# Kernel optimization log

Measured on AMD Instinct MI355X. Metric: run time of the kernel, lower is better.

## Reference

```python
import jax, jax.numpy as jnp
import numpy as np

G = 64        # supervoxel grid per dim (cfg.orig_grid_shape)
CELL = 16     # pixels per grid cell
T = 32        # tile size in px (covers 2x2 cells)
NT = 32       # tiles per dim per shift config
CH = 40       # Conv_trio channels


def setup_inputs() -> dict:
    key = jax.random.key(0)
    ks = jax.random.split(key, 8)
    W = G * CELL
    curr_image = jax.random.normal(ks[0], (W, W), jnp.float32)
    # masks encode per-pixel supervoxel id (pixel belongs to cell floor(px/CELL))
    ids = (jnp.arange(G)[:, None] * G + jnp.arange(G)[None, :]).astype(jnp.float32)
    masks = jnp.repeat(jnp.repeat(ids, CELL, axis=0), CELL, axis=1)[..., None]
    return {
        'curr_image': curr_image,
        'masks': masks,
        'conv1_w': jax.random.normal(ks[1], (3, 3, 1, CH), jnp.float32) * 0.1,
        'conv1_b': jnp.zeros((CH,), jnp.float32),
        'ln1_s': jnp.ones((CH,), jnp.float32),
        'ln1_b': jnp.zeros((CH,), jnp.float32),
        'conv2_w': jax.random.normal(ks[2], (3, 3, CH, CH), jnp.float32) * 0.1,
        'conv2_b': jnp.zeros((CH,), jnp.float32),
        'ln2_s': jnp.ones((CH,), jnp.float32),
        'ln2_b': jnp.zeros((CH,), jnp.float32),
        'dense_w': jax.random.normal(ks[3], ((T // 4) * (T // 4) * CH, 6), jnp.float32) * 0.02,
        'dense_b': jnp.zeros((6,), jnp.float32),
    }


def _tile(a):
    # [W, W, c] -> [NT*NT, T, T, c]
    c = a.shape[-1]
    return a.reshape(NT, T, NT, T, c).transpose(0, 2, 1, 3, 4).reshape(NT * NT, T, T, c)


def _config_tokens(img, masks, ids, sx, sy):
    # shifted tiling: tile (i,j) covers px [T*i + sx*CELL, ...)
    rolled_img = jnp.roll(img, (-sx * CELL, -sy * CELL), (0, 1))
    rolled_msk = jnp.roll(masks, (-sx * CELL, -sy * CELL), (0, 1))
    img_t = _tile(rolled_img)          # [NT*NT, T, T, 1]
    msk_t = _tile(rolled_msk)[..., 0]  # [NT*NT, T, T]
    curr_ids = ids[sx::2, sy::2].reshape(-1)  # [NT*NT]
    filt = (msk_t == curr_ids[:, None, None]).astype(img_t.dtype)
    return img_t * filt[..., None]


def _conv_trio(x, w, b, s, bln):
    y = jax.lax.conv_general_dilated(x, w, (2, 2), 'SAME',
                                     dimension_numbers=('NHWC', 'HWIO', 'NHWC')) + b
    mu = jnp.mean(y, axis=-1, keepdims=True)
    var = jnp.var(y, axis=-1, keepdims=True)
    y = (y - mu) * jax.lax.rsqrt(var + 1e-6) * s + bln
    return jax.nn.gelu(y)


def reference(curr_image, masks, conv1_w, conv1_b, ln1_s, ln1_b,
              conv2_w, conv2_b, ln2_s, ln2_b, dense_w, dense_b):
    img = curr_image[..., None]  # [W, W, 1]
    ids = (jnp.arange(G)[:, None] * G + jnp.arange(G)[None, :]).astype(masks.dtype)
    tokens = jnp.concatenate([
        _config_tokens(img, masks, ids, 0, 0),
        _config_tokens(img, masks, ids, 1, 0),
        _config_tokens(img, masks, ids, 0, 1),
        _config_tokens(img, masks, ids, 1, 1),
    ], axis=0)  # [4*NT*NT, T, T, 1]
    x = _conv_trio(tokens, conv1_w, conv1_b, ln1_s, ln1_b)  # [F, 16, 16, 40]
    x = _conv_trio(x, conv2_w, conv2_b, ln2_s, ln2_b)       # [F, 8, 8, 40]
    x = x.reshape(x.shape[0], -1)
    return x @ dense_w + dense_b  # node embeddings [F, 6]
```

## Files before the change

### kernel.cpp

```cpp
#include <hip/hip_runtime.h>
#include <math.h>

#define CH 40
#define IMW 1024
#define TOKH (9*10*40)
#define W2T_HALVES (48*48*8)
#define Z1_OFF W2T_HALVES
#define OUTC_OFF (Z1_OFF + 40)
#define Y2T 768

typedef _Float16 v8h __attribute__((ext_vector_type(8)));
typedef _Float16 v4h __attribute__((ext_vector_type(4)));
typedef float    v4f __attribute__((ext_vector_type(4)));
typedef float    v2f __attribute__((ext_vector_type(2)));

__device__ __forceinline__ float gelu_fast(float x) {
    float u = 1.5957691216057308f * (x + 0.044715f * x * x * x);
    return x * __builtin_amdgcn_rcpf(1.0f + __expf(-u));
}

__global__ __launch_bounds__(256) void prep_kernel(
    const float* __restrict__ w2,
    const float* __restrict__ b1, const float* __restrict__ s1,
    const float* __restrict__ bb1,
    const float* __restrict__ b2, const float* __restrict__ s2,
    const float* __restrict__ bb2,
    const float* __restrict__ dw, const float* __restrict__ db,
    _Float16* __restrict__ ws)
{
    const int t = threadIdx.x;
    int idx0 = blockIdx.x * 256 + t;
    for (int idx = idx0; idx < W2T_HALVES; idx += gridDim.x * 256) {
        int j   = idx & 7;
        int co  = (idx >> 3) % 48;
        int kgg = idx / (48 * 8);
        int k   = kgg * 8 + j;
        float v = 0.0f;
        if (co < CH && k < 360) {
            int wi = k / 40, ci = k - wi * 40;
            v = w2[(wi * CH + ci) * CH + co];
        }
        ws[idx] = (_Float16)v;
    }
    if (blockIdx.x != 0) return;

    __shared__ float zs[40];
    __shared__ float w2sum[9][40];
    __shared__ float p2l[120];
    __shared__ float red[4][6];

    if (t < 120) p2l[t] = (t < 40) ? b2[t] : (t < 80 ? s2[t - 40] : bb2[t - 80]);

    if (t >= 64 && t < 128) {
        int lane = t - 64;
        bool act = lane < CH;
        float bv = act ? b1[lane] : 0.f;
        float s = bv;
        #pragma unroll
        for (int m = 1; m < 64; m <<= 1) s += __shfl_xor(s, m, 64);
        float mu = s * (1.0f / CH);
        float d = act ? (bv - mu) : 0.f;
        float q = d * d;
        #pragma unroll
        for (int m = 1; m < 64; m <<= 1) q += __shfl_xor(q, m, 64);
        float rs = rsqrtf(q * (1.0f / CH) + 1e-6f);
        if (act) {
            float g = gelu_fast((bv - mu) * rs * s1[lane] + bb1[lane]);
            zs[lane] = g;
            ws[Z1_OFF + lane] = (_Float16)g;
        }
    }
    __syncthreads();

    for (int idx = t; idx < 360; idx += 256) {
        int wi = idx / 40, ch = idx - wi * 40;
        float s = 0.f;
        #pragma unroll
        for (int ci = 0; ci < CH; ci++)
            s += w2[(wi * CH + ci) * CH + ch] * zs[ci];
        w2sum[wi][ch] = s;
    }
    __syncthreads();

    {
        const int m = t >> 2, sub = t & 3;
        const int p = m >> 3, q = m & 7;
        const int co0 = sub * 10;
        float a6[6] = {0.f, 0.f, 0.f, 0.f, 0.f, 0.f};
        if (p >= 4 || q >= 4) {
            const int drmax = (p == 7) ? 2 : 3;
            const int dcmax = (q == 7) ? 2 : 3;
            float vv[10];
            float s_own = 0.f;
            #pragma unroll
            for (int u = 0; u < 10; u++) {
                float v = p2l[co0 + u];
                for (int dr = 0; dr < drmax; dr++)
                    for (int dc = 0; dc < dcmax; dc++)
                        v += w2sum[dr * 3 + dc][co0 + u];
                vv[u] = v; s_own += v;
            }
            s_own += __shfl_xor(s_own, 1, 64);
            s_own += __shfl_xor(s_own, 2, 64);
            float mu = s_own * (1.0f / CH);
            float v_own = 0.f;
            #pragma unroll
            for (int u = 0; u < 10; u++) { float d = vv[u] - mu; v_own += d * d; }
            v_own += __shfl_xor(v_own, 1, 64);
            v_own += __shfl_xor(v_own, 2, 64);
            float rs = rsqrtf(v_own * (1.0f / CH) + 1e-6f);
            const float* wp = &dw[(m * CH + co0) * 6];
            #pragma unroll
            for (int u = 0; u < 10; u++) {
                float gv = gelu_fast((vv[u] - mu) * rs * p2l[40 + co0 + u] + p2l[80 + co0 + u]);
                v2f w01 = *(const v2f*)&wp[u * 6];
                v2f w23 = *(const v2f*)&wp[u * 6 + 2];
                v2f w45 = *(const v2f*)&wp[u * 6 + 4];
                a6[0] += gv * w01[0]; a6[1] += gv * w01[1];
                a6[2] += gv * w23[0]; a6[3] += gv * w23[1];
                a6[4] += gv * w45[0]; a6[5] += gv * w45[1];
            }
        }
        #pragma unroll
        for (int off = 32; off > 0; off >>= 1)
            #pragma unroll
            for (int k = 0; k < 6; k++) a6[k] += __shfl_down(a6[k], off, 64);
        int wv = t >> 6, lane = t & 63;
        if (lane == 0) {
            #pragma unroll
            for (int k = 0; k < 6; k++) red[wv][k] = a6[k];
        }
        __syncthreads();
        if (t == 0) {
            float* oc = (float*)&ws[OUTC_OFF];
            #pragma unroll
            for (int k = 0; k < 6; k++)
                oc[k] = red[0][k] + red[1][k] + red[2][k] + red[3][k] + db[k];
        }
    }
}

__global__ __launch_bounds__(256) void sgn_kernel(
    const float* __restrict__ img,
    const float* __restrict__ w1, const float* __restrict__ b1,
    const float* __restrict__ s1, const float* __restrict__ bb1,
    const float* __restrict__ b2, const float* __restrict__ s2,
    const float* __restrict__ bb2,
    const float* __restrict__ dw,
    const _Float16* __restrict__ ws,
    float* __restrict__ out)
{
    __shared__ __align__(16) unsigned char sbuf[2 * TOKH * 2];
    _Float16* x1h = (_Float16*)sbuf;
    float*    y2f = (float*)sbuf;
    __shared__ float img_s[2][16][16];
    __shared__ float w1t[40 * 12];
    __shared__ float p1s[120];
    __shared__ float p2s[120];
    __shared__ unsigned koff_s[48];

    const int t = threadIdx.x;

    int crr[2], ccc[2];
    #pragma unroll
    for (int tk = 0; tk < 2; tk++) {
        int f   = blockIdx.x * 2 + tk;
        int cfg = f >> 10;
        int ij  = f & 1023;
        int ti  = ij >> 5, tj = ij & 31;
        crr[tk] = 2 * ti + (cfg & 1);
        ccc[tk] = 2 * tj + (cfg >> 1);
    }

    {
        int r = t >> 4, c = t & 15;
        #pragma unroll
        for (int tk = 0; tk < 2; tk++)
            img_s[tk][r][c] = img[(crr[tk] * 16 + r) * IMW + ccc[tk] * 16 + c];
    }
    for (int i = t; i < 360; i += 256) {
        int k = i / 40, ch = i - k * 40;
        w1t[ch * 12 + k] = w1[i];
    }
    if (t < 120) {
        p1s[t] = (t < 40) ? b1[t] : (t < 80 ? s1[t - 40] : bb1[t - 80]);
    } else if (t >= 128 && t < 248) {
        int i = t - 128;
        p2s[i] = (i < 40) ? b2[i] : (i < 80 ? s2[i - 40] : bb2[i - 80]);
    }
    if (t < 48) {
        int s = t >> 2, kg = t & 3;
        int k0 = 32 * s + 8 * kg;
        unsigned v = 0;
        if (k0 < 360) {
            int wi = k0 / 40, ci0 = k0 - wi * 40;
            int dr = wi / 3, dc = wi - 3 * dr;
            v = (unsigned)((dr * 10 + dc) * 40 + ci0);
        }
        koff_s[t] = v;
    }
    __syncthreads();

    {
        const int tk  = t >> 7;
        const int pos = (t >> 1) & 63;
        const int sub = t & 1;
        const int r = pos >> 3, c = pos & 7;
        float vin[9];
        #pragma unroll
        for (int dr = 0; dr < 3; dr++)
            #pragma unroll
            for (int dc = 0; dc < 3; dc++) {
                int rr = 2 * r + dr, cp = 2 * c + dc;
                vin[dr * 3 + dc] = (rr < 16 && cp < 16) ? img_s[tk][rr][cp] : 0.0f;
            }
        const int ch0 = sub * 20;
        float y[20];
        float s_own = 0.f;
        #pragma unroll
        for (int u = 0; u < 20; u++) {
            float a = p1s[ch0 + u];
            const float* wr = &w1t[(ch0 + u) * 12];
            #pragma unroll
            for (int k = 0; k < 9; k++) a += vin[k] * wr[k];
            y[u] = a; s_own += a;
        }
        s_own += __shfl_xor(s_own, 1, 64);
        float mu = s_own * (1.0f / CH);
        float v_own = 0.f;
        #pragma unroll
        for (int u = 0; u < 20; u++) { float d = y[u] - mu; v_own += d * d; }
        v_own += __shfl_xor(v_own, 1, 64);
        float rs = rsqrtf(v_own * (1.0f / CH) + 1e-6f);
        _Float16 g[20];
        #pragma unroll
        for (int u = 0; u < 20; u++) {
            int ch = ch0 + u;
            g[u] = (_Float16)gelu_fast((y[u] - mu) * rs * p1s[40 + ch] + p1s[80 + ch]);
        }
        const int base = tk * TOKH + (r * 10 + c) * 40 + ch0;
        if (sub == 0) {
            *(v8h*)&x1h[base]      = *(v8h*)&g[0];
            *(v8h*)&x1h[base + 8]  = *(v8h*)&g[8];
            *(v4h*)&x1h[base + 16] = *(v4h*)&g[16];
        } else {
            *(v4h*)&x1h[base]      = *(v4h*)&g[0];
            *(v8h*)&x1h[base + 4]  = *(v8h*)&g[4];
            *(v8h*)&x1h[base + 12] = *(v8h*)&g[12];
        }
    }
    if (t < 34) {
        int tk = (t >= 17), i = t - tk * 17;
        int r = (i < 9) ? 8 : (i - 9);
        int c = (i < 9) ? i : 8;
        const v8h* zsrc = (const v8h*)&ws[Z1_OFF];
        int base = tk * TOKH + (r * 10 + c) * 40;
        *(v8h*)&x1h[base]      = zsrc[0];
        *(v8h*)&x1h[base + 8]  = zsrc[1];
        *(v8h*)&x1h[base + 16] = zsrc[2];
        *(v8h*)&x1h[base + 24] = zsrc[3];
        *(v8h*)&x1h[base + 32] = zsrc[4];
    }
    __syncthreads();

    v4f accA = {0,0,0,0}, accB = {0,0,0,0};
    const int wv   = t >> 6;
    const int lane = t & 63;
    if (wv < 3) {
        const int row = lane & 15;
        const int kg  = lane >> 4;
        const unsigned pbase = (unsigned)((20 * (row >> 2) + 2 * (row & 3)) * 40);
        #pragma unroll
        for (int s = 0; s < 12; s++) {
            const int kc = (s << 2) | kg;
            unsigned aoff = pbase + koff_s[kc];
            v8h a0 = *(const v8h*)&x1h[aoff];
            v8h a1 = *(const v8h*)&x1h[TOKH + aoff];
            v8h bf = *(const v8h*)&ws[(kc * 48 + wv * 16 + row) * 8];
            accA = __builtin_amdgcn_mfma_f32_16x16x32_f16(a0, bf, accA, 0, 0, 0);
            accB = __builtin_amdgcn_mfma_f32_16x16x32_f16(a1, bf, accB, 0, 0, 0);
        }
    }
    __syncthreads();

    if (wv < 3) {
        const int cix = lane & 15;
        const int kg  = lane >> 4;
        if (wv < 2 || cix < 8) {
            #pragma unroll
            for (int j = 0; j < 4; j++) {
                int m = (kg << 2) | j;
                y2f[m * 48 + wv * 16 + cix]       = accA[j];
                y2f[Y2T + m * 48 + wv * 16 + cix] = accB[j];
            }
        }
    }
    __syncthreads();

    if (t < 128) {
        const int tk  = t >> 6;
        const int pos = (t >> 2) & 15;
        const int sub = t & 3;
        const int co0 = sub * 10;
        float vv[10];
        float s_own = 0.f;
        #pragma unroll
        for (int u = 0; u < 10; u++) {
            float a = y2f[tk * Y2T + pos * 48 + co0 + u] + p2s[co0 + u];
            vv[u] = a; s_own += a;
        }
        s_own += __shfl_xor(s_own, 1, 64);
        s_own += __shfl_xor(s_own, 2, 64);
        float mu = s_own * (1.0f / CH);
        float v_own = 0.f;
        #pragma unroll
        for (int u = 0; u < 10; u++) { float d = vv[u] - mu; v_own += d * d; }
        v_own += __shfl_xor(v_own, 1, 64);
        v_own += __shfl_xor(v_own, 2, 64);
        float rs = rsqrtf(v_own * (1.0f / CH) + 1e-6f);

        const int p = pos >> 2, q = pos & 3;
        const float* wp = &dw[((p * 8 + q) * CH + co0) * 6];
        float a6[6] = {0.f, 0.f, 0.f, 0.f, 0.f, 0.f};
        #pragma unroll
        for (int u = 0; u < 10; u++) {
            float gv = gelu_fast((vv[u] - mu) * rs * p2s[40 + co0 + u] + p2s[80 + co0 + u]);
            v2f w01 = *(const v2f*)&wp[u * 6];
            v2f w23 = *(const v2f*)&wp[u * 6 + 2];
            v2f w45 = *(const v2f*)&wp[u * 6 + 4];
            a6[0] += gv * w01[0]; a6[1] += gv * w01[1];
            a6[2] += gv * w23[0]; a6[3] += gv * w23[1];
            a6[4] += gv * w45[0]; a6[5] += gv * w45[1];
        }
        #pragma unroll
        for (int off = 32; off > 0; off >>= 1)
            #pragma unroll
            for (int k = 0; k < 6; k++) a6[k] += __shfl_down(a6[k], off, 64);
        if (lane == 0) {
            const float* oc = (const float*)&ws[OUTC_OFF];
            int f = blockIdx.x * 2 + tk;
            #pragma unroll
            for (int k = 0; k < 6; k++) out[f * 6 + k] = a6[k] + oc[k];
        }
    }
}

extern "C" void kernel_launch(void* const* d_in, const int* in_sizes, int n_in,
                              void* d_out, int out_size, void* d_ws, size_t ws_size,
                              hipStream_t stream) {
    const float* img = (const float*)d_in[0];
    const float* w1  = (const float*)d_in[2];
    const float* b1  = (const float*)d_in[3];
    const float* s1  = (const float*)d_in[4];
    const float* bb1 = (const float*)d_in[5];
    const float* w2  = (const float*)d_in[6];
    const float* b2  = (const float*)d_in[7];
    const float* s2  = (const float*)d_in[8];
    const float* bb2 = (const float*)d_in[9];
    const float* dw  = (const float*)d_in[10];
    const float* db  = (const float*)d_in[11];
    float* out = (float*)d_out;
    _Float16* ws = (_Float16*)d_ws;

    prep_kernel<<<32, 256, 0, stream>>>(w2, b1, s1, bb1, b2, s2, bb2, dw, db, ws);
    sgn_kernel<<<2048, 256, 0, stream>>>(img, w1, b1, s1, bb1,
                                         b2, s2, bb2, dw, ws, out);
}
```

Baseline: 32.21 us.

## Process one token per single-wavefront block with register-resident epilogue

Changes sgn_kernel from 256-thread blocks handling two tokens to 64-thread blocks, one wavefront per token. Each lane now computes all 40 conv1 channels for one output pixel and reads the image straight from global memory instead of staging it in LDS. That wave then issues three MFMAs per K step, one per output-channel group. The conv2 LayerNorm, GELU and dense epilogue work directly on the MFMA accumulators using cross-lane shuffles, which drops the LDS round trip and two block barriers. In exchange, each lane holds more registers (40-channel arrays) and per-block setup (weight and parameter loads into LDS) is repeated twice as often.

```diff
diff --git a/kernel.cpp b/kernel.cpp
--- a/kernel.cpp
+++ b/kernel.cpp
@@ -7,10 +7,8 @@
 #define W2T_HALVES (48*48*8)
 #define Z1_OFF W2T_HALVES
 #define OUTC_OFF (Z1_OFF + 40)
-#define Y2T 768
 
 typedef _Float16 v8h __attribute__((ext_vector_type(8)));
-typedef _Float16 v4h __attribute__((ext_vector_type(4)));
 typedef float    v4f __attribute__((ext_vector_type(4)));
 typedef float    v2f __attribute__((ext_vector_type(2)));
 
@@ -140,7 +138,7 @@
     }
 }
 
-__global__ __launch_bounds__(256) void sgn_kernel(
+__global__ __launch_bounds__(64) void sgn_kernel(
     const float* __restrict__ img,
     const float* __restrict__ w1, const float* __restrict__ b1,
     const float* __restrict__ s1, const float* __restrict__ bb1,
@@ -150,111 +148,83 @@
     const _Float16* __restrict__ ws,
     float* __restrict__ out)
 {
-    __shared__ __align__(16) unsigned char sbuf[2 * TOKH * 2];
-    _Float16* x1h = (_Float16*)sbuf;
-    float*    y2f = (float*)sbuf;
-    __shared__ float img_s[2][16][16];
+    __shared__ __align__(16) _Float16 x1h[TOKH];
     __shared__ float w1t[40 * 12];
     __shared__ float p1s[120];
     __shared__ float p2s[120];
     __shared__ unsigned koff_s[48];
 
-    const int t = threadIdx.x;
-
-    int crr[2], ccc[2];
-    #pragma unroll
-    for (int tk = 0; tk < 2; tk++) {
-        int f   = blockIdx.x * 2 + tk;
-        int cfg = f >> 10;
-        int ij  = f & 1023;
-        int ti  = ij >> 5, tj = ij & 31;
-        crr[tk] = 2 * ti + (cfg & 1);
-        ccc[tk] = 2 * tj + (cfg >> 1);
-    }
-
-    {
-        int r = t >> 4, c = t & 15;
-        #pragma unroll
-        for (int tk = 0; tk < 2; tk++)
-            img_s[tk][r][c] = img[(crr[tk] * 16 + r) * IMW + ccc[tk] * 16 + c];
-    }
-    for (int i = t; i < 360; i += 256) {
+    const int lane = threadIdx.x;
+    const int f   = blockIdx.x;
+    const int cfg = f >> 10;
+    const int ij  = f & 1023;
+    const int ti  = ij >> 5, tj = ij & 31;
+    const int cr  = 2 * ti + (cfg & 1);
+    const int cc  = 2 * tj + (cfg >> 1);
+
+    for (int i = lane; i < 360; i += 64) {
         int k = i / 40, ch = i - k * 40;
         w1t[ch * 12 + k] = w1[i];
     }
-    if (t < 120) {
-        p1s[t] = (t < 40) ? b1[t] : (t < 80 ? s1[t - 40] : bb1[t - 80]);
-    } else if (t >= 128 && t < 248) {
-        int i = t - 128;
+    for (int i = lane; i < 120; i += 64)
+        p1s[i] = (i < 40) ? b1[i] : (i < 80 ? s1[i - 40] : bb1[i - 80]);
+    for (int i = lane; i < 120; i += 64)
         p2s[i] = (i < 40) ? b2[i] : (i < 80 ? s2[i - 40] : bb2[i - 80]);
-    }
-    if (t < 48) {
-        int s = t >> 2, kg = t & 3;
-        int k0 = 32 * s + 8 * kg;
+    if (lane < 48) {
+        int k0 = 8 * lane;
         unsigned v = 0;
         if (k0 < 360) {
             int wi = k0 / 40, ci0 = k0 - wi * 40;
             int dr = wi / 3, dc = wi - 3 * dr;
             v = (unsigned)((dr * 10 + dc) * 40 + ci0);
         }
-        koff_s[t] = v;
+        koff_s[lane] = v;
     }
     __syncthreads();
 
     {
-        const int tk  = t >> 7;
-        const int pos = (t >> 1) & 63;
-        const int sub = t & 1;
-        const int r = pos >> 3, c = pos & 7;
+        const int r = lane >> 3, c = lane & 7;
+        const float* ib = &img[(cr * 16) * IMW + cc * 16];
         float vin[9];
         #pragma unroll
         for (int dr = 0; dr < 3; dr++)
             #pragma unroll
             for (int dc = 0; dc < 3; dc++) {
                 int rr = 2 * r + dr, cp = 2 * c + dc;
-                vin[dr * 3 + dc] = (rr < 16 && cp < 16) ? img_s[tk][rr][cp] : 0.0f;
+                vin[dr * 3 + dc] = (rr < 16 && cp < 16) ? ib[rr * IMW + cp] : 0.0f;
             }
-        const int ch0 = sub * 20;
-        float y[20];
-        float s_own = 0.f;
-        #pragma unroll
-        for (int u = 0; u < 20; u++) {
-            float a = p1s[ch0 + u];
-            const float* wr = &w1t[(ch0 + u) * 12];
+        float y[40];
+        float s = 0.f;
+        #pragma unroll
+        for (int ch = 0; ch < 40; ch++) {
+            float a = p1s[ch];
+            const float* wr = &w1t[ch * 12];
             #pragma unroll
             for (int k = 0; k < 9; k++) a += vin[k] * wr[k];
-            y[u] = a; s_own += a;
-        }
-        s_own += __shfl_xor(s_own, 1, 64);
-        float mu = s_own * (1.0f / CH);
-        float v_own = 0.f;
-        #pragma unroll
-        for (int u = 0; u < 20; u++) { float d = y[u] - mu; v_own += d * d; }
-        v_own += __shfl_xor(v_own, 1, 64);
-        float rs = rsqrtf(v_own * (1.0f / CH) + 1e-6f);
-        _Float16 g[20];
-        #pragma unroll
-        for (int u = 0; u < 20; u++) {
-            int ch = ch0 + u;
-            g[u] = (_Float16)gelu_fast((y[u] - mu) * rs * p1s[40 + ch] + p1s[80 + ch]);
-        }
-        const int base = tk * TOKH + (r * 10 + c) * 40 + ch0;
-        if (sub == 0) {
-            *(v8h*)&x1h[base]      = *(v8h*)&g[0];
-            *(v8h*)&x1h[base + 8]  = *(v8h*)&g[8];
-            *(v4h*)&x1h[base + 16] = *(v4h*)&g[16];
-        } else {
-            *(v4h*)&x1h[base]      = *(v4h*)&g[0];
-            *(v8h*)&x1h[base + 4]  = *(v8h*)&g[4];
-            *(v8h*)&x1h[base + 12] = *(v8h*)&g[12];
-        }
-    }
-    if (t < 34) {
-        int tk = (t >= 17), i = t - tk * 17;
-        int r = (i < 9) ? 8 : (i - 9);
-        int c = (i < 9) ? i : 8;
+            y[ch] = a; s += a;
+        }
+        float mu = s * (1.0f / CH);
+        float q = 0.f;
+        #pragma unroll
+        for (int ch = 0; ch < 40; ch++) { float d = y[ch] - mu; q += d * d; }
+        float rs = rsqrtf(q * (1.0f / CH) + 1e-6f);
+        const int base = (r * 10 + c) * 40;
+        #pragma unroll
+        for (int chk = 0; chk < 5; chk++) {
+            v8h hv;
+            #pragma unroll
+            for (int jj = 0; jj < 8; jj++) {
+                int ch = chk * 8 + jj;
+                hv[jj] = (_Float16)gelu_fast((y[ch] - mu) * rs * p1s[40 + ch] + p1s[80 + ch]);
+            }
+            *(v8h*)&x1h[base + chk * 8] = hv;
+        }
+    }
+    if (lane < 17) {
+        int rr = (lane < 9) ? 8 : (lane - 9);
+        int cb = (lane < 9) ? lane : 8;
         const v8h* zsrc = (const v8h*)&ws[Z1_OFF];
-        int base = tk * TOKH + (r * 10 + c) * 40;
+        int base = (rr * 10 + cb) * 40;
         *(v8h*)&x1h[base]      = zsrc[0];
         *(v8h*)&x1h[base + 8]  = zsrc[1];
         *(v8h*)&x1h[base + 16] = zsrc[2];
@@ -263,74 +233,62 @@
     }
     __syncthreads();
 
-    v4f accA = {0,0,0,0}, accB = {0,0,0,0};
-    const int wv   = t >> 6;
-    const int lane = t & 63;
-    if (wv < 3) {
-        const int row = lane & 15;
-        const int kg  = lane >> 4;
+    v4f acc0 = {0,0,0,0}, acc1 = {0,0,0,0}, acc2 = {0,0,0,0};
+    const int row = lane & 15;
+    const int kg  = lane >> 4;
+    {
         const unsigned pbase = (unsigned)((20 * (row >> 2) + 2 * (row & 3)) * 40);
         #pragma unroll
         for (int s = 0; s < 12; s++) {
             const int kc = (s << 2) | kg;
             unsigned aoff = pbase + koff_s[kc];
-            v8h a0 = *(const v8h*)&x1h[aoff];
-            v8h a1 = *(const v8h*)&x1h[TOKH + aoff];
-            v8h bf = *(const v8h*)&ws[(kc * 48 + wv * 16 + row) * 8];
-            accA = __builtin_amdgcn_mfma_f32_16x16x32_f16(a0, bf, accA, 0, 0, 0);
-            accB = __builtin_amdgcn_mfma_f32_16x16x32_f16(a1, bf, accB, 0, 0, 0);
-        }
-    }
-    __syncthreads();
-
-    if (wv < 3) {
-        const int cix = lane & 15;
-        const int kg  = lane >> 4;
-        if (wv < 2 || cix < 8) {
-            #pragma unroll
-            for (int j = 0; j < 4; j++) {
-                int m = (kg << 2) | j;
-                y2f[m * 48 + wv * 16 + cix]       = accA[j];
-                y2f[Y2T + m * 48 + wv * 16 + cix] = accB[j];
-            }
-        }
-    }
-    __syncthreads();
-
-    if (t < 128) {
-        const int tk  = t >> 6;
-        const int pos = (t >> 2) & 15;
-        const int sub = t & 3;
-        const int co0 = sub * 10;
-        float vv[10];
-        float s_own = 0.f;
-        #pragma unroll
-        for (int u = 0; u < 10; u++) {
-            float a = y2f[tk * Y2T + pos * 48 + co0 + u] + p2s[co0 + u];
-            vv[u] = a; s_own += a;
-        }
-        s_own += __shfl_xor(s_own, 1, 64);
-        s_own += __shfl_xor(s_own, 2, 64);
-        float mu = s_own * (1.0f / CH);
-        float v_own = 0.f;
-        #pragma unroll
-        for (int u = 0; u < 10; u++) { float d = vv[u] - mu; v_own += d * d; }
-        v_own += __shfl_xor(v_own, 1, 64);
-        v_own += __shfl_xor(v_own, 2, 64);
-        float rs = rsqrtf(v_own * (1.0f / CH) + 1e-6f);
-
-        const int p = pos >> 2, q = pos & 3;
-        const float* wp = &dw[((p * 8 + q) * CH + co0) * 6];
+            v8h a = *(const v8h*)&x1h[aoff];
+            const _Float16* wb = &ws[(kc * 48 + row) * 8];
+            v8h bf0 = *(const v8h*)&wb[0];
+            v8h bf1 = *(const v8h*)&wb[16 * 8];
+            v8h bf2 = *(const v8h*)&wb[32 * 8];
+            acc0 = __builtin_amdgcn_mfma_f32_16x16x32_f16(a, bf0, acc0, 0, 0, 0);
+            acc1 = __builtin_amdgcn_mfma_f32_16x16x32_f16(a, bf1, acc1, 0, 0, 0);
+            acc2 = __builtin_amdgcn_mfma_f32_16x16x32_f16(a, bf2, acc2, 0, 0, 0);
+        }
+    }
+
+    {
+        const int cix = row;
+        const bool h2 = (cix < 8);
+        const float b2a = p2s[cix],      b2b = p2s[16 + cix],      b2c = h2 ? p2s[32 + cix] : 0.f;
+        const float s2a = p2s[40 + cix], s2b = p2s[56 + cix],      s2c = h2 ? p2s[72 + cix] : 0.f;
+        const float g2a = p2s[80 + cix], g2b = p2s[96 + cix],      g2c = h2 ? p2s[112 + cix] : 0.f;
         float a6[6] = {0.f, 0.f, 0.f, 0.f, 0.f, 0.f};
         #pragma unroll
-        for (int u = 0; u < 10; u++) {
-            float gv = gelu_fast((vv[u] - mu) * rs * p2s[40 + co0 + u] + p2s[80 + co0 + u]);
-            v2f w01 = *(const v2f*)&wp[u * 6];
-            v2f w23 = *(const v2f*)&wp[u * 6 + 2];
-            v2f w45 = *(const v2f*)&wp[u * 6 + 4];
-            a6[0] += gv * w01[0]; a6[1] += gv * w01[1];
-            a6[2] += gv * w23[0]; a6[3] += gv * w23[1];
-            a6[4] += gv * w45[0]; a6[5] += gv * w45[1];
+        for (int j = 0; j < 4; j++) {
+            const int m = (kg << 2) | j;
+            float v0 = acc0[j] + b2a;
+            float v1 = acc1[j] + b2b;
+            float v2 = h2 ? (acc2[j] + b2c) : 0.f;
+            float s = v0 + v1 + v2;
+            s += __shfl_xor(s, 1, 64);
+            s += __shfl_xor(s, 2, 64);
+            s += __shfl_xor(s, 4, 64);
+            s += __shfl_xor(s, 8, 64);
+            float mu = s * (1.0f / CH);
+            float d0 = v0 - mu, d1 = v1 - mu, d2 = v2 - mu;
+            float q = d0 * d0 + d1 * d1 + (h2 ? d2 * d2 : 0.f);
+            q += __shfl_xor(q, 1, 64);
+            q += __shfl_xor(q, 2, 64);
+            q += __shfl_xor(q, 4, 64);
+            q += __shfl_xor(q, 8, 64);
+            float rs = rsqrtf(q * (1.0f / CH) + 1e-6f);
+            float g0 = gelu_fast(d0 * rs * s2a + g2a);
+            float g1 = gelu_fast(d1 * rs * s2b + g2b);
+            float g2 = h2 ? gelu_fast(d2 * rs * s2c + g2c) : 0.f;
+            const int drow = ((m >> 2) * 8 + (m & 3)) * CH;
+            const float* w0p = &dw[(drow + cix) * 6];
+            const float* w1p = &dw[(drow + 16 + cix) * 6];
+            const float* w2p = &dw[(drow + 32 + cix) * 6];
+            #pragma unroll
+            for (int k = 0; k < 6; k++)
+                a6[k] += g0 * w0p[k] + g1 * w1p[k] + g2 * w2p[k];
         }
         #pragma unroll
         for (int off = 32; off > 0; off >>= 1)
@@ -338,7 +296,6 @@
             for (int k = 0; k < 6; k++) a6[k] += __shfl_down(a6[k], off, 64);
         if (lane == 0) {
             const float* oc = (const float*)&ws[OUTC_OFF];
-            int f = blockIdx.x * 2 + tk;
             #pragma unroll
             for (int k = 0; k < 6; k++) out[f * 6 + k] = a6[k] + oc[k];
         }
@@ -363,6 +320,6 @@
     _Float16* ws = (_Float16*)d_ws;
 
     prep_kernel<<<32, 256, 0, stream>>>(w2, b1, s1, bb1, b2, s2, bb2, dw, db, ws);
-    sgn_kernel<<<2048, 256, 0, stream>>>(img, w1, b1, s1, bb1,
-                                         b2, s2, bb2, dw, ws, out);
+    sgn_kernel<<<4096, 64, 0, stream>>>(img, w1, b1, s1, bb1,
+                                        b2, s2, bb2, dw, ws, out);
 }
```

Result: slower. 36.36 us (+12.9%).
